# Kernel optimization log

Measured on AMD Instinct MI355X. Metric: run time of the kernel, lower is better.

Reference implementation:

```python
import jax, jax.numpy as jnp
import numpy as np
from jax import lax

N = 8192  # total_nodes


def setup_inputs() -> dict:
    key = jax.random.key(0)
    kx, kW = jax.random.split(key)
    x = jax.random.normal(kx, (2,), dtype=jnp.float32)
    W = jax.random.normal(kW, (N, N), dtype=jnp.float32) * 0.1
    b = jnp.zeros((N,), dtype=jnp.float32)
    return {"x": x, "W": W, "b": b}


def reference(x, W, b):
    # Sequential DAG scan: s[j] = sigmoid(sum_{i<j} W[i,j] * s[i] + b[j])
    # (triu mask with diagonal=1 is all-ones over the slice [:j, j])
    n = W.shape[0]
    idx = jnp.arange(n)
    s0 = jnp.zeros((n,), dtype=W.dtype).at[0].set(x[0]).at[1].set(x[1])

    def step(s, j):
        m = (idx < j).astype(s.dtype)          # strict-upper-triangular mask column
        ws = jnp.sum(W[:, j] * m * s)          # weighted sum over predecessors
        val = jax.nn.sigmoid(ws + b[j])
        return s.at[j].set(val), None

    s, _ = lax.scan(step, s0, jnp.arange(2, n))
    return s[n - 1]
```

## Files before the change

### kernel.cpp

```cpp
#include <hip/hip_runtime.h>

#define NN 8192
#define SBS 512
#define NSB 16
#define LOG2E 1.44269504088896f

#define FR(k,w) (32 + ((k)*8 + (w))*32)
#define PART_OFF 8192
#define CP_OFF   16384
#define SARR_OFF 81920

__device__ __forceinline__ float bcastf(float v, int lane) {
    return __int_as_float(__builtin_amdgcn_readlane(__float_as_int(v), lane));
}
__device__ __forceinline__ float sigm(float prelog) {
    return __builtin_amdgcn_rcpf(1.0f + __builtin_amdgcn_exp2f(-prelog));
}
__device__ __forceinline__ int ld_flag(const int* p) {
    return __hip_atomic_load(p, __ATOMIC_RELAXED, __HIP_MEMORY_SCOPE_AGENT);
}
__device__ __forceinline__ void st_rel(int* p, int v) {
    __hip_atomic_store(p, v, __ATOMIC_RELEASE, __HIP_MEMORY_SCOPE_AGENT);
}
__device__ __forceinline__ float ldf(const float* p) {
    return __hip_atomic_load(p, __ATOMIC_RELAXED, __HIP_MEMORY_SCOPE_AGENT);
}
__device__ __forceinline__ void stf(float* p, float v) {
    __hip_atomic_store(p, v, __ATOMIC_RELAXED, __HIP_MEMORY_SCOPE_AGENT);
}
#define LBAR() do { asm volatile("s_waitcnt lgkmcnt(0)\ns_barrier" ::: "memory"); \
                    __builtin_amdgcn_sched_barrier(0); } while (0)

__global__ void init_ws(int* wsi, float* wsf) {
    int i = blockIdx.x * 256 + threadIdx.x;
    if (i < 8192) wsi[i] = 0;
    if (i < 65536) wsf[CP_OFF + i] = 0.0f;
}

template <int TW>
__device__ void helper_fn(const float* __restrict__ W, float* wsf, int* flags,
                          float (*red)[8][64], int k) {
    const int tid = threadIdx.x, g = tid >> 6, l = tid & 63;
    float* partials = wsf + PART_OFF;
    const float* s_arr = wsf + SARR_OFF;
    const int J0 = k * SBS;

    float pr[TW - 1][8];
    #pragma unroll
    for (int m = 0; m < TW - 1; ++m)
        #pragma unroll
        for (int r = 0; r < 8; ++r)
            pr[m][r] = W[(size_t)(J0 + m*64 + g*8 + r) * NN + (J0 + TW*64 + l)];

    float part = 0.0f;
    #pragma unroll
    for (int m = 0; m <= TW - 2; ++m) {
        if (tid < 64) {
            while (ld_flag(&flags[0]) < k*8 + m + 1) __builtin_amdgcn_s_sleep(2);
        }
        __syncthreads();
        __builtin_amdgcn_fence(__ATOMIC_ACQUIRE, "agent");
        #pragma unroll
        for (int r = 0; r < 8; ++r)
            part += pr[m][r] * ldf(&s_arr[J0 + m*64 + g*8 + r]);
    }
    red[0][g][l] = part;
    __syncthreads();
    if (tid < 64) {
        float tot = 0.0f;
        #pragma unroll
        for (int g2 = 0; g2 < 8; ++g2) tot += red[0][g2][tid];
        stf(&partials[((size_t)k*8 + TW)*64 + tid], tot);
    }
    __syncthreads();
    if (tid == 0) st_rel(&flags[FR(k, TW)], 1);
}

__device__ void solver_fn(const float* __restrict__ W, const float* __restrict__ b,
                          const float* __restrict__ x, float* wsf, int* flags,
                          float* sdiag, float* spub, float* sacc,
                          float (*red)[8][64], float* __restrict__ out, int k) {
    const int tid = threadIdx.x;
    const int w = tid >> 6, l = tid & 63;
    const int dj = tid >> 3, dc = (tid & 7) * 8;
    const int J0 = k * SBS;
    const float* cp = wsf + CP_OFF;
    float* partials = wsf + PART_OFF;
    float* s_arr = wsf + SARR_OFF;

    auto load_diag = [&](int mm, float4& a, float4& bq) {
        const float* p = &W[(size_t)(J0 + mm*64 + dj) * NN + (J0 + mm*64 + dc)];
        a  = *(const float4*)p;
        bq = *(const float4*)(p + 4);
    };
    auto write_diag = [&](int mm, float4 a, float4 bq) {
        float* dst = &sdiag[mm*4096 + dj*64 + dc];
        float v[8] = {a.x, a.y, a.z, a.w, bq.x, bq.y, bq.z, bq.w};
        #pragma unroll
        for (int e = 0; e < 8; ++e) dst[e] = (dj < dc + e) ? v[e] * LOG2E : 0.0f;
    };
    auto load_panel = [&](int mm, float* pr) {
        #pragma unroll
        for (int r = 0; r < 8; ++r)
            pr[r] = W[(size_t)(J0 + mm*64 + w*8 + r) * NN + (J0 + (mm+1)*64 + l)];
    };

    const float x0 = x[0], x1 = x[1];
    float base = b[J0 + tid];
    #pragma unroll
    for (int r = 0; r < 8; ++r) base += cp[r * NN + J0 + tid];
    float4 dA[2], dB[2];
    load_diag(0, dA[0], dB[0]);
    load_diag(1, dA[1], dB[1]);
    float preg[2][8];
    load_panel(0, preg[0]);
    load_panel(1, preg[1]);
    write_diag(0, dA[0], dB[0]);
    write_diag(1, dA[1], dB[1]);
    sacc[tid] = base;
    LBAR();

    #pragma unroll
    for (int m = 0; m < 8; ++m) {
        if (w == m) {
            float part = 0.0f;
            if (m >= 2) {
                const int* fl = &flags[FR(k, m)];
                while (ld_flag(fl) == 0) {}
                __builtin_amdgcn_fence(__ATOMIC_ACQUIRE, "agent");
                part = ldf(&partials[((size_t)k*8 + m)*64 + l]);
            }
            float rsum = 0.0f;
            if (m >= 1) {
                #pragma unroll
                for (int g = 0; g < 8; ++g) rsum += red[(m-1) & 1][g][l];
            }
            float acc = (sacc[m*64 + l] + rsum + part) * LOG2E;
            float smine = 0.0f;
            const bool first = (k == 0) && (m == 0);
            #pragma unroll
            for (int j = 0; j < 64; ++j) {
                const float pre = bcastf(acc, j);
                float s;
                if (first && j == 0)      s = x0;
                else if (first && j == 1) s = x1;
                else                      s = sigm(pre);
                acc += sdiag[m*4096 + j*64 + l] * s;
                if (l == j) smine = s;
            }
            spub[m*64 + l] = smine;
            stf(&s_arr[J0 + m*64 + l], smine);
            if (k == NSB - 1 && m == 7 && l == 63) out[0] = smine;
            if (l == 0) st_rel(&flags[0], k*8 + m + 1);
        }
        LBAR();
        if (m < 7) {
            float partial = 0.0f;
            #pragma unroll
            for (int r = 0; r < 8; ++r)
                partial += preg[m & 1][r] * spub[m*64 + w*8 + r];
            red[m & 1][w][l] = partial;
            if (m >= 1) write_diag(m + 1, dA[(m+1) & 1], dB[(m+1) & 1]);
            if (m + 2 <= 7) load_diag(m + 2, dA[(m+2) & 1], dB[(m+2) & 1]);
            if (m + 2 <= 6) load_panel(m + 2, preg[m & 1]);
            LBAR();
        }
    }
}

__global__ void __launch_bounds__(512, 1) solve_kernel(
    const float* __restrict__ W, const float* __restrict__ b,
    const float* __restrict__ x, float* wsf, int* flags,
    float* __restrict__ out, int k)
{
    __shared__ float sdiag[8 * 4096];
    __shared__ float spub[512];
    __shared__ float sacc[512];
    __shared__ float red[2][8][64];
    const int bid = blockIdx.x;
    if (bid == 0) {
        solver_fn(W, b, x, wsf, flags, sdiag, spub, sacc, red, out, k);
    } else {
        switch (bid) {
            case 1: helper_fn<2>(W, wsf, flags, red, k); break;
            case 2: helper_fn<3>(W, wsf, flags, red, k); break;
            case 3: helper_fn<4>(W, wsf, flags, red, k); break;
            case 4: helper_fn<5>(W, wsf, flags, red, k); break;
            case 5: helper_fn<6>(W, wsf, flags, red, k); break;
            case 6: helper_fn<7>(W, wsf, flags, red, k); break;
        }
    }
}

__global__ void __launch_bounds__(256) update_kernel(
    const float* __restrict__ W, const float* __restrict__ wsf_s,
    float* __restrict__ cp, int k)
{
    __shared__ float ssh[64];
    const int tid = threadIdx.x;
    const int rc = blockIdx.y;
    const int row0 = k * SBS + rc * 64;
    const int col = (k + 1) * SBS + blockIdx.x * 256 + tid;
    if (tid < 64) ssh[tid] = wsf_s[row0 + tid];
    __syncthreads();
    const float* wp = W + (size_t)row0 * NN + col;
    float a0 = 0.f, a1 = 0.f, a2 = 0.f, a3 = 0.f;
    #pragma unroll
    for (int i = 0; i < 64; i += 4) {
        a0 += wp[(size_t)(i + 0) * NN] * ssh[i + 0];
        a1 += wp[(size_t)(i + 1) * NN] * ssh[i + 1];
        a2 += wp[(size_t)(i + 2) * NN] * ssh[i + 2];
        a3 += wp[(size_t)(i + 3) * NN] * ssh[i + 3];
    }
    cp[rc * NN + col] += (a0 + a1) + (a2 + a3);
}

extern "C" void kernel_launch(void* const* d_in, const int* in_sizes, int n_in,
                              void* d_out, int out_size, void* d_ws, size_t ws_size,
                              hipStream_t stream) {
    const float* x = (const float*)d_in[0];
    const float* W = (const float*)d_in[1];
    const float* b = (const float*)d_in[2];
    float* out = (float*)d_out;
    float* wsf = (float*)d_ws;
    int* wsi   = (int*)d_ws;
    float* cp    = wsf + CP_OFF;
    float* s_arr = wsf + SARR_OFF;

    init_ws<<<dim3(256), dim3(256), 0, stream>>>(wsi, wsf);
    for (int k = 0; k < NSB; ++k) {
        solve_kernel<<<dim3(7), dim3(512), 0, stream>>>(W, b, x, wsf, wsi, out, k);
        if (k < NSB - 1) {
            int M = NN - (k + 1) * SBS;
            update_kernel<<<dim3(M / 256, 8), dim3(256), 0, stream>>>(W, s_arr, cp, k);
        }
    }
}
```

Baseline: 422.0 us.

## Fuse lagged trailing update into solver launch with near-column helper blocks

Removes the separate update kernel. Each per-superblock launch now also runs two kinds of extra blocks. Near blocks compute the current superblock's contribution to the next superblock's columns as soon as s values are published. Bulk blocks apply the previous superblock's contribution to all later columns, running concurrently with the solver. The solver also takes over the distance-2 panel locally, so the helper set shrinks. The aim is to halve the number of launches and hide the trailing GEMV behind the serial solve, at the cost of an extra cp row, more solver registers and more spin-waiting blocks.

```diff
diff --git a/kernel.cpp b/kernel.cpp
--- a/kernel.cpp
+++ b/kernel.cpp
@@ -8,7 +8,8 @@
 #define FR(k,w) (32 + ((k)*8 + (w))*32)
 #define PART_OFF 8192
 #define CP_OFF   16384
-#define SARR_OFF 81920
+#define NCPROW   9
+#define SARR_OFF (CP_OFF + NCPROW * NN)
 
 __device__ __forceinline__ float bcastf(float v, int lane) {
     return __int_as_float(__builtin_amdgcn_readlane(__float_as_int(v), lane));
@@ -34,52 +35,14 @@
 __global__ void init_ws(int* wsi, float* wsf) {
     int i = blockIdx.x * 256 + threadIdx.x;
     if (i < 8192) wsi[i] = 0;
-    if (i < 65536) wsf[CP_OFF + i] = 0.0f;
-}
-
-template <int TW>
-__device__ void helper_fn(const float* __restrict__ W, float* wsf, int* flags,
-                          float (*red)[8][64], int k) {
-    const int tid = threadIdx.x, g = tid >> 6, l = tid & 63;
-    float* partials = wsf + PART_OFF;
-    const float* s_arr = wsf + SARR_OFF;
-    const int J0 = k * SBS;
-
-    float pr[TW - 1][8];
-    #pragma unroll
-    for (int m = 0; m < TW - 1; ++m)
-        #pragma unroll
-        for (int r = 0; r < 8; ++r)
-            pr[m][r] = W[(size_t)(J0 + m*64 + g*8 + r) * NN + (J0 + TW*64 + l)];
-
-    float part = 0.0f;
-    #pragma unroll
-    for (int m = 0; m <= TW - 2; ++m) {
-        if (tid < 64) {
-            while (ld_flag(&flags[0]) < k*8 + m + 1) __builtin_amdgcn_s_sleep(2);
-        }
-        __syncthreads();
-        __builtin_amdgcn_fence(__ATOMIC_ACQUIRE, "agent");
-        #pragma unroll
-        for (int r = 0; r < 8; ++r)
-            part += pr[m][r] * ldf(&s_arr[J0 + m*64 + g*8 + r]);
-    }
-    red[0][g][l] = part;
-    __syncthreads();
-    if (tid < 64) {
-        float tot = 0.0f;
-        #pragma unroll
-        for (int g2 = 0; g2 < 8; ++g2) tot += red[0][g2][tid];
-        stf(&partials[((size_t)k*8 + TW)*64 + tid], tot);
-    }
-    __syncthreads();
-    if (tid == 0) st_rel(&flags[FR(k, TW)], 1);
+    wsf[CP_OFF + i] = 0.0f;
 }
 
 __device__ void solver_fn(const float* __restrict__ W, const float* __restrict__ b,
                           const float* __restrict__ x, float* wsf, int* flags,
                           float* sdiag, float* spub, float* sacc,
-                          float (*red)[8][64], float* __restrict__ out, int k) {
+                          float (*redN)[8][64], float (*redF)[8][64],
+                          float* __restrict__ out, int k) {
     const int tid = threadIdx.x;
     const int w = tid >> 6, l = tid & 63;
     const int dj = tid >> 3, dc = (tid & 7) * 8;
@@ -99,32 +62,40 @@
         #pragma unroll
         for (int e = 0; e < 8; ++e) dst[e] = (dj < dc + e) ? v[e] * LOG2E : 0.0f;
     };
-    auto load_panel = [&](int mm, float* pr) {
+    auto load_pan1 = [&](int mm, float* pr) {
         #pragma unroll
         for (int r = 0; r < 8; ++r)
             pr[r] = W[(size_t)(J0 + mm*64 + w*8 + r) * NN + (J0 + (mm+1)*64 + l)];
+    };
+    auto load_pan2 = [&](int mm, float* pr) {
+        #pragma unroll
+        for (int r = 0; r < 8; ++r)
+            pr[r] = W[(size_t)(J0 + mm*64 + w*8 + r) * NN + (J0 + (mm+2)*64 + l)];
     };
 
     const float x0 = x[0], x1 = x[1];
     float base = b[J0 + tid];
     #pragma unroll
-    for (int r = 0; r < 8; ++r) base += cp[r * NN + J0 + tid];
+    for (int r = 0; r < NCPROW; ++r) base += cp[r * NN + J0 + tid];
     float4 dA[2], dB[2];
     load_diag(0, dA[0], dB[0]);
     load_diag(1, dA[1], dB[1]);
-    float preg[2][8];
-    load_panel(0, preg[0]);
-    load_panel(1, preg[1]);
+    float p1[2][8], p2[2][8];
+    load_pan1(0, p1[0]);
+    load_pan1(1, p1[1]);
+    load_pan2(0, p2[0]);
+    load_pan2(1, p2[1]);
     write_diag(0, dA[0], dB[0]);
     write_diag(1, dA[1], dB[1]);
     sacc[tid] = base;
+    redF[1][w][l] = 0.0f;
     LBAR();
 
     #pragma unroll
     for (int m = 0; m < 8; ++m) {
         if (w == m) {
             float part = 0.0f;
-            if (m >= 2) {
+            if (m >= 3) {
                 const int* fl = &flags[FR(k, m)];
                 while (ld_flag(fl) == 0) {}
                 __builtin_amdgcn_fence(__ATOMIC_ACQUIRE, "agent");
@@ -133,7 +104,11 @@
             float rsum = 0.0f;
             if (m >= 1) {
                 #pragma unroll
-                for (int g = 0; g < 8; ++g) rsum += red[(m-1) & 1][g][l];
+                for (int g = 0; g < 8; ++g) rsum += redN[m & 1][g][l];
+            }
+            if (m >= 2) {
+                #pragma unroll
+                for (int g = 0; g < 8; ++g) rsum += redF[m & 1][g][l];
             }
             float acc = (sacc[m*64 + l] + rsum + part) * LOG2E;
             float smine = 0.0f;
@@ -155,20 +130,126 @@
         }
         LBAR();
         if (m < 7) {
-            float partial = 0.0f;
+            float f1 = 0.0f;
             #pragma unroll
             for (int r = 0; r < 8; ++r)
-                partial += preg[m & 1][r] * spub[m*64 + w*8 + r];
-            red[m & 1][w][l] = partial;
+                f1 += p1[m & 1][r] * spub[m*64 + w*8 + r];
+            redN[(m+1) & 1][w][l] = f1;
+            if (m < 6) {
+                float f2 = 0.0f;
+                #pragma unroll
+                for (int r = 0; r < 8; ++r)
+                    f2 += p2[m & 1][r] * spub[m*64 + w*8 + r];
+                redF[m & 1][w][l] = f2;
+            }
             if (m >= 1) write_diag(m + 1, dA[(m+1) & 1], dB[(m+1) & 1]);
             if (m + 2 <= 7) load_diag(m + 2, dA[(m+2) & 1], dB[(m+2) & 1]);
-            if (m + 2 <= 6) load_panel(m + 2, preg[m & 1]);
+            if (m + 2 <= 6) load_pan1(m + 2, p1[m & 1]);
+            if (m + 2 <= 5) load_pan2(m + 2, p2[m & 1]);
             LBAR();
         }
     }
 }
 
-__global__ void __launch_bounds__(512, 1) solve_kernel(
+template <int TW>
+__device__ void helper_fn(const float* __restrict__ W, float* wsf, int* flags,
+                          float (*redh)[64], int k) {
+    const int tid = threadIdx.x, g = tid >> 6, l = tid & 63;
+    float* partials = wsf + PART_OFF;
+    const float* s_arr = wsf + SARR_OFF;
+    const int J0 = k * SBS;
+
+    float pr[TW - 2][8];
+    #pragma unroll
+    for (int m = 0; m <= TW - 3; ++m)
+        #pragma unroll
+        for (int r = 0; r < 8; ++r)
+            pr[m][r] = W[(size_t)(J0 + m*64 + g*8 + r) * NN + (J0 + TW*64 + l)];
+
+    float part = 0.0f;
+    #pragma unroll
+    for (int m = 0; m <= TW - 3; ++m) {
+        if (tid < 64) {
+            while (ld_flag(&flags[0]) < k*8 + m + 1) __builtin_amdgcn_s_sleep(2);
+        }
+        __syncthreads();
+        __builtin_amdgcn_fence(__ATOMIC_ACQUIRE, "agent");
+        #pragma unroll
+        for (int r = 0; r < 8; ++r)
+            part += pr[m][r] * ldf(&s_arr[J0 + m*64 + g*8 + r]);
+    }
+    redh[g][l] = part;
+    __syncthreads();
+    if (tid < 64) {
+        float tot = 0.0f;
+        #pragma unroll
+        for (int g2 = 0; g2 < 8; ++g2) tot += redh[g2][tid];
+        stf(&partials[((size_t)k*8 + TW)*64 + tid], tot);
+    }
+    __syncthreads();
+    if (tid == 0) st_rel(&flags[FR(k, TW)], 1);
+}
+
+__device__ void near_fn(const float* __restrict__ W, float* wsf, int* flags,
+                        float (*redh)[64], int t, int k) {
+    const int tid = threadIdx.x, g = tid >> 6, l = tid & 63;
+    const int col = (k+1)*SBS + t*64 + l;
+    const float* s_arr = wsf + SARR_OFF;
+    float* cp = wsf + CP_OFF;
+
+    float pr[8][8];
+    #pragma unroll
+    for (int m = 0; m < 8; ++m)
+        #pragma unroll
+        for (int r = 0; r < 8; ++r)
+            pr[m][r] = W[(size_t)(k*SBS + m*64 + g*8 + r) * NN + col];
+
+    float part = 0.0f;
+    #pragma unroll
+    for (int m = 0; m < 8; ++m) {
+        if (tid < 64) {
+            while (ld_flag(&flags[0]) < k*8 + m + 1) __builtin_amdgcn_s_sleep(4);
+        }
+        __syncthreads();
+        __builtin_amdgcn_fence(__ATOMIC_ACQUIRE, "agent");
+        #pragma unroll
+        for (int r = 0; r < 8; ++r)
+            part += pr[m][r] * ldf(&s_arr[k*SBS + m*64 + g*8 + r]);
+    }
+    redh[g][l] = part;
+    __syncthreads();
+    if (g == 0) {
+        float tot = 0.0f;
+        #pragma unroll
+        for (int g2 = 0; g2 < 8; ++g2) tot += redh[g2][l];
+        cp[8 * NN + col] = tot;
+    }
+}
+
+__device__ void bulk_fn(const float* __restrict__ W, float* wsf,
+                        float* ssh, int idx, int k) {
+    const int tid = threadIdx.x;
+    const int rc = idx & 7, cg = idx >> 3;
+    const int row0 = (k-1)*SBS + rc*64;
+    const int col = (k+1)*SBS + cg*SBS + tid;
+    const float* s_arr = wsf + SARR_OFF;
+    float* cp = wsf + CP_OFF;
+
+    if (tid < 64) ssh[tid] = s_arr[row0 + tid];
+    __syncthreads();
+    const float* wp = W + (size_t)row0 * NN + col;
+    float a0 = 0.f, a1 = 0.f, a2 = 0.f, a3 = 0.f;
+    #pragma unroll
+    for (int i = 0; i < 64; i += 4) {
+        a0 += wp[(size_t)(i + 0) * NN] * ssh[i + 0];
+        a1 += wp[(size_t)(i + 1) * NN] * ssh[i + 1];
+        a2 += wp[(size_t)(i + 2) * NN] * ssh[i + 2];
+        a3 += wp[(size_t)(i + 3) * NN] * ssh[i + 3];
+    }
+    cp[rc * NN + col] += (a0 + a1) + (a2 + a3);
+}
+
+__global__ void __launch_bounds__(512, 1) mega_kernel(
     const float* __restrict__ W, const float* __restrict__ b,
     const float* __restrict__ x, float* wsf, int* flags,
     float* __restrict__ out, int k)
@@ -176,43 +257,25 @@
     __shared__ float sdiag[8 * 4096];
     __shared__ float spub[512];
     __shared__ float sacc[512];
-    __shared__ float red[2][8][64];
+    __shared__ float redN[2][8][64];
+    __shared__ float redF[2][8][64];
+    __shared__ float redh[8][64];
     const int bid = blockIdx.x;
     if (bid == 0) {
-        solver_fn(W, b, x, wsf, flags, sdiag, spub, sacc, red, out, k);
+        solver_fn(W, b, x, wsf, flags, sdiag, spub, sacc, redN, redF, out, k);
+    } else if (bid <= 5) {
+        switch (bid) {
+            case 1: helper_fn<3>(W, wsf, flags, redh, k); break;
+            case 2: helper_fn<4>(W, wsf, flags, redh, k); break;
+            case 3: helper_fn<5>(W, wsf, flags, redh, k); break;
+            case 4: helper_fn<6>(W, wsf, flags, redh, k); break;
+            case 5: helper_fn<7>(W, wsf, flags, redh, k); break;
+        }
+    } else if (bid <= 13) {
+        near_fn(W, wsf, flags, redh, bid - 6, k);
     } else {
-        switch (bid) {
-            case 1: helper_fn<2>(W, wsf, flags, red, k); break;
-            case 2: helper_fn<3>(W, wsf, flags, red, k); break;
-            case 3: helper_fn<4>(W, wsf, flags, red, k); break;
-            case 4: helper_fn<5>(W, wsf, flags, red, k); break;
-            case 5: helper_fn<6>(W, wsf, flags, red, k); break;
-            case 6: helper_fn<7>(W, wsf, flags, red, k); break;
-        }
-    }
-}
-
-__global__ void __launch_bounds__(256) update_kernel(
-    const float* __restrict__ W, const float* __restrict__ wsf_s,
-    float* __restrict__ cp, int k)
-{
-    __shared__ float ssh[64];
-    const int tid = threadIdx.x;
-    const int rc = blockIdx.y;
-    const int row0 = k * SBS + rc * 64;
-    const int col = (k + 1) * SBS + blockIdx.x * 256 + tid;
-    if (tid < 64) ssh[tid] = wsf_s[row0 + tid];
-    __syncthreads();
-    const float* wp = W + (size_t)row0 * NN + col;
-    float a0 = 0.f, a1 = 0.f, a2 = 0.f, a3 = 0.f;
-    #pragma unroll
-    for (int i = 0; i < 64; i += 4) {
-        a0 += wp[(size_t)(i + 0) * NN] * ssh[i + 0];
-        a1 += wp[(size_t)(i + 1) * NN] * ssh[i + 1];
-        a2 += wp[(size_t)(i + 2) * NN] * ssh[i + 2];
-        a3 += wp[(size_t)(i + 3) * NN] * ssh[i + 3];
-    }
-    cp[rc * NN + col] += (a0 + a1) + (a2 + a3);
+        bulk_fn(W, wsf, &redh[0][0], bid - 14, k);
+    }
 }
 
 extern "C" void kernel_launch(void* const* d_in, const int* in_sizes, int n_in,
@@ -224,15 +287,13 @@
     float* out = (float*)d_out;
     float* wsf = (float*)d_ws;
     int* wsi   = (int*)d_ws;
-    float* cp    = wsf + CP_OFF;
-    float* s_arr = wsf + SARR_OFF;
-
-    init_ws<<<dim3(256), dim3(256), 0, stream>>>(wsi, wsf);
+
+    init_ws<<<dim3(288), dim3(256), 0, stream>>>(wsi, wsf);
     for (int k = 0; k < NSB; ++k) {
-        solve_kernel<<<dim3(7), dim3(512), 0, stream>>>(W, b, x, wsf, wsi, out, k);
-        if (k < NSB - 1) {
-            int M = NN - (k + 1) * SBS;
-            update_kernel<<<dim3(M / 256, 8), dim3(256), 0, stream>>>(W, s_arr, cp, k);
-        }
-    }
-}
+        int nb;
+        if (k == 0)            nb = 14;
+        else if (k == NSB - 1) nb = 6;
+        else                   nb = 14 + (15 - k) * 8;
+        mega_kernel<<<dim3(nb), dim3(512), 0, stream>>>(W, b, x, wsf, wsi, out, k);
+    }
+}
```

Result: faster. 411.7 us (-2.4%).
